# Kernel tuning notes

Hardware: AMD Instinct MI355X
Metric: run time of the kernel (lower is better)

Reference implementation:

```python
import jax, jax.numpy as jnp
import numpy as np

N_HEADS = 16

def setup_inputs() -> dict:
    key = jax.random.key(0)
    k1, k2, k3, k4, k5 = jax.random.split(key, 5)
    B, S, D = 2, 2048, 1024
    x = jax.random.normal(k1, (B, S, D), dtype=jnp.float32)
    # parameters scaled ~ fan-in to keep softmax logits sane
    w_in = jax.random.normal(k2, (D, 3 * D), dtype=jnp.float32) * (1.0 / np.sqrt(D))
    b_in = jax.random.normal(k3, (3 * D,), dtype=jnp.float32) * 0.02
    w_out = jax.random.normal(k4, (D, D), dtype=jnp.float32) * (1.0 / np.sqrt(D))
    b_out = jax.random.normal(k5, (D,), dtype=jnp.float32) * 0.02
    return {"x": x, "w_in": w_in, "b_in": b_in, "w_out": w_out, "b_out": b_out,
            "causal_mask": 1}


def reference(x, w_in, b_in, w_out, b_out, causal_mask):
    B, S, D = x.shape
    H = N_HEADS
    dh = D // H
    qkv = x @ w_in + b_in                        # [B, S, 3D]
    q, k, v = jnp.split(qkv, 3, axis=-1)          # each [B, S, D]
    q = q.reshape(B, S, H, dh)
    k = k.reshape(B, S, H, dh)
    v = v.reshape(B, S, H, dh)
    # scores: [B, H, Sq, Sk]
    scores = jnp.einsum("bqhd,bkhd->bhqk", q, k)
    if causal_mask:
        mask = jnp.triu(jnp.ones((S, S), dtype=bool), k=1)
        scores = jnp.where(mask, -jnp.inf, scores)
    scores = scores / jnp.sqrt(jnp.asarray(dh, dtype=scores.dtype))
    weight = jax.nn.softmax(scores, axis=-1)
    out = jnp.einsum("bhqk,bkhd->bqhd", weight, v).reshape(B, S, D)
    return out @ w_out + b_out
```

## Files before the change

### kernel.cpp

```cpp
#include <hip/hip_runtime.h>
#include <hip/hip_bf16.h>

typedef __attribute__((ext_vector_type(8))) short short8;
typedef __attribute__((ext_vector_type(4))) short s16x4;
typedef __attribute__((ext_vector_type(4))) float f32x4;
typedef unsigned short u16;

__device__ inline u16 f2bf(float f) {
    union { float f; unsigned u; } x{f};
    unsigned r = (x.u + 0x7fff + ((x.u >> 16) & 1)) >> 16;
    return (u16)r;
}

__device__ inline unsigned pkbf(float hi, float lo) {
    unsigned a = __builtin_bit_cast(unsigned, hi) + 0x8000u;
    unsigned b = __builtin_bit_cast(unsigned, lo) + 0x8000u;
    return __builtin_amdgcn_perm(a, b, 0x07060302u);
}

__device__ inline void glds16(const u16* g, u16* l) {
    __builtin_amdgcn_global_load_lds(
        (const __attribute__((address_space(1))) void*)g,
        (__attribute__((address_space(3))) void*)l, 16, 0, 0);
}

__global__ __launch_bounds__(256) void prep(const float* __restrict__ x,
                                            const float* __restrict__ w_in,
                                            const float* __restrict__ w_out,
                                            u16* __restrict__ Xb,
                                            u16* __restrict__ WtIn,
                                            u16* __restrict__ WtOut) {
    __shared__ float tile[32][33];
    int bx = blockIdx.x, tid = threadIdx.x;
    if (bx < 4096) {
        int i = (bx * 256 + tid) * 4;
        float4 v = *(const float4*)&x[i];
        uint2 o;
        o.x = (unsigned)f2bf(v.x) | ((unsigned)f2bf(v.y) << 16);
        o.y = (unsigned)f2bf(v.z) | ((unsigned)f2bf(v.w) << 16);
        *(uint2*)&Xb[i] = o;
        return;
    }
    const float* W; u16* Wt; int K, N, n0, k0;
    if (bx < 7168) {
        int b2 = bx - 4096;
        W = w_in; Wt = WtIn; K = 1024; N = 3072;
        n0 = (b2 % 96) * 32; k0 = (b2 / 96) * 32;
    } else {
        int b3 = bx - 7168;
        W = w_out; Wt = WtOut; K = 1024; N = 1024;
        n0 = (b3 & 31) * 32; k0 = (b3 >> 5) * 32;
    }
    int tx = tid & 31, ty = tid >> 5;
    for (int i = 0; i < 32; i += 8)
        tile[ty + i][tx] = W[(size_t)(k0 + ty + i) * N + n0 + tx];
    __syncthreads();
    for (int i = 0; i < 32; i += 8)
        Wt[(size_t)(n0 + ty + i) * K + k0 + tx] = f2bf(tile[tx][ty + i]);
}

__global__ __launch_bounds__(256) void transpose_v(const u16* __restrict__ qkv,
                                                   u16* __restrict__ VT) {
    __shared__ u16 t[32][33];
    int s0 = blockIdx.x * 32, d0 = blockIdx.y * 32, bh = blockIdx.z;
    int b = bh >> 4, h = bh & 15;
    int tx = threadIdx.x, ty = threadIdx.y;
    const u16* Vp = qkv + (size_t)(b * 2048) * 3072 + 2048 + h * 64;
    for (int i = 0; i < 32; i += 8)
        t[ty + i][tx] = Vp[(size_t)(s0 + ty + i) * 3072 + d0 + tx];
    __syncthreads();
    u16* Vr = VT + (size_t)bh * 64 * 2048;
    for (int i = 0; i < 32; i += 8)
        Vr[(size_t)(d0 + ty + i) * 2048 + s0 + tx] = t[tx][ty + i];
}

#define BM 128
#define BN 128
#define BK 64
__global__ __launch_bounds__(256) void gemm_bt(const u16* __restrict__ A,
                                               const u16* __restrict__ Bt,
                                               const float* __restrict__ bias,
                                               void* __restrict__ C,
                                               int M, int N, int K, int c_is_f32,
                                               int qcols, float qscale) {
    __shared__ u16 smem[2 * BM * BK + 2048];
    u16* As = smem;
    u16* Bs = smem + BM * BK;

    int tid = threadIdx.x;
    int wave = tid >> 6, lane = tid & 63;
    int quad = lane >> 4, l16 = lane & 15;
    int wm = (wave >> 1) * 64, wn = (wave & 1) * 64;

    int nm = M / BM, nn = N / BN;
    const int GM = 8;
    int per_group = GM * nn;
    int group = blockIdx.x / per_group;
    int rem = blockIdx.x % per_group;
    int first_m = group * GM;
    int gsz = (nm - first_m < GM) ? (nm - first_m) : GM;
    int m0 = (first_m + rem % gsz) * BM;
    int n0 = (rem / gsz) * BN;

    f32x4 acc[4][4] = {};

    for (int k0 = 0; k0 < K; k0 += BK) {
        __syncthreads();
        for (int i = 0; i < 4; i++) {
            int c = tid + i * 256;
            int r = c >> 3, cc = c & 7;
            int gsrc = (cc ^ (r & 7)) * 8;
            glds16(&A[(size_t)(m0 + r) * K + k0 + gsrc], As + c * 8);
            glds16(&Bt[(size_t)(n0 + r) * K + k0 + gsrc], Bs + c * 8);
        }
        __syncthreads();
        for (int ks = 0; ks < 2; ks++) {
            short8 af[4], bf[4];
            for (int i = 0; i < 4; i++) {
                int row = wm + i * 16 + l16;
                int slot = (ks * 4 + quad) ^ (row & 7);
                af[i] = *(short8*)&As[row * BK + slot * 8];
            }
            for (int j = 0; j < 4; j++) {
                int row = wn + j * 16 + l16;
                int slot = (ks * 4 + quad) ^ (row & 7);
                bf[j] = *(short8*)&Bs[row * BK + slot * 8];
            }
            for (int i = 0; i < 4; i++)
                for (int j = 0; j < 4; j++)
                    acc[i][j] = __builtin_amdgcn_mfma_f32_16x16x32_bf16(
                        af[i], bf[j], acc[i][j], 0, 0, 0);
        }
    }

    if (c_is_f32) {
        for (int i = 0; i < 4; i++)
            for (int j = 0; j < 4; j++) {
                int col = n0 + wn + j * 16 + l16;
                float bv = bias ? bias[col] : 0.f;
                for (int r = 0; r < 4; r++) {
                    int row = m0 + wm + i * 16 + quad * 4 + r;
                    ((float*)C)[(size_t)row * N + col] = acc[i][j][r] + bv;
                }
            }
    } else {
        __syncthreads();
        u16 (*buf)[136] = (u16(*)[136])smem;
        for (int i = 0; i < 4; i++)
            for (int j = 0; j < 4; j++) {
                int col = wn + j * 16 + l16;
                float bv = bias ? bias[n0 + col] : 0.f;
                float scl = (n0 + col < qcols) ? qscale : 1.f;
                for (int r = 0; r < 4; r++)
                    buf[wm + i * 16 + quad * 4 + r][col] =
                        f2bf((acc[i][j][r] + bv) * scl);
            }
        __syncthreads();
        u16* Cb = (u16*)C;
        for (int it = 0; it < 8; it++) {
            int c = tid + it * 256;
            int row = c >> 4, k8 = c & 15;
            uint4 v = *(uint4*)&buf[row][k8 * 8];
            *(uint4*)&Cb[(size_t)(m0 + row) * N + n0 + k8 * 8] = v;
        }
    }
}

__global__ __launch_bounds__(512) void attn_kernel(const u16* __restrict__ qkv,
                                                   const u16* __restrict__ VT,
                                                   u16* __restrict__ out) {
    const int S = 2048, D = 1024, stride = 3072;
    int idx = blockIdx.x;
    int p = idx >> 5, bh = idx & 31;
    int qtb[2] = {15 - p, p};
    int b = bh >> 4, h = bh & 15;
    int tid = threadIdx.x;
    int wave = tid >> 6, lane = tid & 63;
    int quad = lane >> 4, l16 = lane & 15;

    __shared__ u16 Klds[2][64 * 64];
    __shared__ u16 Vlds[2][64 * 64];
    __shared__ u16 Obuf[8][16][72];

    const u16* Qp = qkv + (size_t)(b * S) * stride + h * 64;
    const u16* Kp = Qp + D;
    const u16* Vtp = VT + (size_t)bh * 64 * S;

    short8 qf[2][2];
    for (int ph = 0; ph < 2; ph++) {
        int qrow = qtb[ph] * 128 + wave * 16 + l16;
        qf[ph][0] = *(const short8*)&Qp[(size_t)qrow * stride + quad * 8];
        qf[ph][1] = *(const short8*)&Qp[(size_t)qrow * stride + 32 + quad * 8];
    }

    int nt0 = 2 * qtb[0] + 2;
    int total = nt0 + 2 * qtb[1] + 2;

    auto stage = [&](int kt, int bsel) {
        int c = tid;
        int r = c >> 3, cc = c & 7;
        int gsrc = (cc ^ (r & 7)) * 8;
        glds16(&Kp[(size_t)(kt * 64 + r) * stride + gsrc], &Klds[bsel][c * 8]);
        glds16(&Vtp[(size_t)r * S + kt * 64 + gsrc], &Vlds[bsel][c * 8]);
    };

    stage(0, 0);

    f32x4 O[4] = {};
    float lsum = 0.f;

    for (int it = 0; it < total; it++) {
        int ph = (it >= nt0) ? 1 : 0;
        int kt = ph ? it - nt0 : it;
        int qt = qtb[ph];
        int cur = it & 1;
        __syncthreads();
        if (it + 1 < total) {
            int it2 = it + 1;
            int k2 = (it2 >= nt0) ? it2 - nt0 : it2;
            stage(k2, cur ^ 1);
        }

        short8 kf[4][2];
        for (int nb = 0; nb < 4; nb++) {
            int r = nb * 16 + l16;
            kf[nb][0] = *(short8*)&Klds[cur][r * 64 + ((0 + quad) ^ (r & 7)) * 8];
            kf[nb][1] = *(short8*)&Klds[cur][r * 64 + ((4 + quad) ^ (r & 7)) * 8];
        }
        f32x4 st[4];
        for (int nb = 0; nb < 4; nb++) {
            f32x4 t = {};
            t = __builtin_amdgcn_mfma_f32_16x16x32_bf16(kf[nb][0], qf[ph][0], t, 0, 0, 0);
            t = __builtin_amdgcn_mfma_f32_16x16x32_bf16(kf[nb][1], qf[ph][1], t, 0, 0, 0);
            st[nb] = t;
        }

        if (kt >= 2 * qt) {
            int qabs = qt * 128 + wave * 16 + l16;
            for (int nb = 0; nb < 4; nb++) {
                int kb = kt * 64 + nb * 16 + quad * 4;
                for (int r = 0; r < 4; r++) {
                    float e = __builtin_amdgcn_exp2f(st[nb][r]);
                    st[nb][r] = (kb + r <= qabs) ? e : 0.f;
                }
            }
        } else {
            for (int nb = 0; nb < 4; nb++)
                for (int r = 0; r < 4; r++)
                    st[nb][r] = __builtin_amdgcn_exp2f(st[nb][r]);
        }

        s16x4 pf[4];
        for (int nb = 0; nb < 4; nb++) {
            lsum += (st[nb][0] + st[nb][1]) + (st[nb][2] + st[nb][3]);
            uint2 pk;
            pk.x = pkbf(st[nb][1], st[nb][0]);
            pk.y = pkbf(st[nb][3], st[nb][2]);
            pf[nb] = __builtin_bit_cast(s16x4, pk);
        }

        for (int db = 0; db < 4; db++) {
            int rr = db * 16 + l16;
            for (int kc = 0; kc < 4; kc++) {
                int g = kc * 2 + (quad >> 1);
                int slot = g ^ (rr & 7);
                s16x4 vf = *(s16x4*)&Vlds[cur][rr * 64 + slot * 8 + (quad & 1) * 4];
                O[db] = __builtin_amdgcn_mfma_f32_16x16x16bf16_1k(
                    pf[kc], vf, O[db], 0, 0, 0);
            }
        }

        if (it == nt0 - 1 || it == total - 1) {
            float v = lsum;
            v += __shfl_xor(v, 16);
            v += __shfl_xor(v, 32);
            float rinv[4];
            for (int r = 0; r < 4; r++)
                rinv[r] = 1.f / __shfl(v, (lane & 48) | (quad * 4 + r));
            for (int db = 0; db < 4; db++)
                for (int r = 0; r < 4; r++)
                    Obuf[wave][quad * 4 + r][db * 16 + l16] =
                        f2bf(O[db][r] * rinv[r]);
            __asm__ volatile("s_waitcnt lgkmcnt(0)" ::: "memory");
            for (int i = 0; i < 2; i++) {
                int c = i * 64 + lane;
                int row = c >> 3, cc = c & 7;
                uint4 vv = *(uint4*)&Obuf[wave][row][cc * 8];
                int grow = qt * 128 + wave * 16 + row;
                *(uint4*)&out[(size_t)(b * S + grow) * D + h * 64 + cc * 8] = vv;
            }
            for (int db = 0; db < 4; db++) O[db] = (f32x4){0.f, 0.f, 0.f, 0.f};
            lsum = 0.f;
        }
    }
}

extern "C" void kernel_launch(void* const* d_in, const int* in_sizes, int n_in,
                              void* d_out, int out_size, void* d_ws, size_t ws_size,
                              hipStream_t stream) {
    const float* x     = (const float*)d_in[0];
    const float* w_in  = (const float*)d_in[1];
    const float* b_in  = (const float*)d_in[2];
    const float* w_out = (const float*)d_in[3];
    const float* b_out = (const float*)d_in[4];

    const int Bsz = 2, S = 2048, D = 1024, H = 16;
    const int M = Bsz * S;
    const int N1 = 3 * D;
    const float sc = 0.125f * 1.44269504f;

    u16* ws    = (u16*)d_ws;
    u16* Xb    = ws;
    u16* WtIn  = Xb + (size_t)M * D;
    u16* WtOut = WtIn + (size_t)N1 * D;
    u16* qkvb  = WtOut + (size_t)D * D;
    u16* attnb = qkvb + (size_t)M * N1;
    u16* Vt    = Xb;

    prep<<<8192, 256, 0, stream>>>(x, w_in, w_out, Xb, WtIn, WtOut);
    gemm_bt<<<(M / BM) * (N1 / BN), 256, 0, stream>>>(Xb, WtIn, b_in, qkvb,
                                                      M, N1, D, 0, D, sc);
    transpose_v<<<dim3(S / 32, 2, Bsz * H), dim3(32, 8), 0, stream>>>(qkvb, Vt);
    attn_kernel<<<256, 512, 0, stream>>>(qkvb, Vt, attnb);
    gemm_bt<<<(M / BM) * (D / BN), 256, 0, stream>>>(attnb, WtOut, b_out, d_out,
                                                     M, D, D, 1, 0, 1.f);
}
```

Before: 192.1 us.

## Process two K/V tiles per iteration in attention with dual accumulators

The attention loop now stages and consumes two 64-key tiles per iteration, using separate score, probability and output accumulators for each tile, and sums them at the end. This halves the number of barriers and gives the scheduler two independent MFMA chains to interleave, which should hide latency. It also adds a minimum-occupancy hint to launch bounds. The cost is doubled LDS (64KB+ for K/V) and more registers, which could lower occupancy or cause spills.

```diff
diff --git a/kernel.cpp b/kernel.cpp
--- a/kernel.cpp
+++ b/kernel.cpp
@@ -166,9 +166,9 @@
     }
 }
 
-__global__ __launch_bounds__(512) void attn_kernel(const u16* __restrict__ qkv,
-                                                   const u16* __restrict__ VT,
-                                                   u16* __restrict__ out) {
+__global__ __launch_bounds__(512, 2) void attn_kernel(const u16* __restrict__ qkv,
+                                                      const u16* __restrict__ VT,
+                                                      u16* __restrict__ out) {
     const int S = 2048, D = 1024, stride = 3072;
     int idx = blockIdx.x;
     int p = idx >> 5, bh = idx & 31;
@@ -178,8 +178,8 @@
     int wave = tid >> 6, lane = tid & 63;
     int quad = lane >> 4, l16 = lane & 15;
 
-    __shared__ u16 Klds[2][64 * 64];
-    __shared__ u16 Vlds[2][64 * 64];
+    __shared__ u16 Klds[2][2][64 * 64];
+    __shared__ u16 Vlds[2][2][64 * 64];
     __shared__ u16 Obuf[8][16][72];
 
     const u16* Qp = qkv + (size_t)(b * S) * stride + h * 64;
@@ -193,70 +193,90 @@
         qf[ph][1] = *(const short8*)&Qp[(size_t)qrow * stride + 32 + quad * 8];
     }
 
-    int nt0 = 2 * qtb[0] + 2;
-    int total = nt0 + 2 * qtb[1] + 2;
-
-    auto stage = [&](int kt, int bsel) {
+    int np0 = qtb[0] + 1;
+    int ntp = np0 + qtb[1] + 1;
+
+    auto stage = [&](int kt, int bsel, int ch) {
         int c = tid;
         int r = c >> 3, cc = c & 7;
         int gsrc = (cc ^ (r & 7)) * 8;
-        glds16(&Kp[(size_t)(kt * 64 + r) * stride + gsrc], &Klds[bsel][c * 8]);
-        glds16(&Vtp[(size_t)r * S + kt * 64 + gsrc], &Vlds[bsel][c * 8]);
+        glds16(&Kp[(size_t)(kt * 64 + r) * stride + gsrc], &Klds[bsel][ch][c * 8]);
+        glds16(&Vtp[(size_t)r * S + kt * 64 + gsrc], &Vlds[bsel][ch][c * 8]);
     };
 
-    stage(0, 0);
-
-    f32x4 O[4] = {};
-    float lsum = 0.f;
-
-    for (int it = 0; it < total; it++) {
-        int ph = (it >= nt0) ? 1 : 0;
-        int kt = ph ? it - nt0 : it;
+    stage(0, 0, 0);
+    stage(1, 0, 1);
+
+    f32x4 Oa[4] = {}, Ob[4] = {};
+    float lsa = 0.f, lsb = 0.f;
+
+    for (int jp = 0; jp < ntp; jp++) {
+        int ph = (jp >= np0) ? 1 : 0;
+        int j = ph ? jp - np0 : jp;
         int qt = qtb[ph];
-        int cur = it & 1;
-        __syncthreads();
-        if (it + 1 < total) {
-            int it2 = it + 1;
-            int k2 = (it2 >= nt0) ? it2 - nt0 : it2;
-            stage(k2, cur ^ 1);
-        }
-
-        short8 kf[4][2];
+        int ka = 2 * j, kb = 2 * j + 1;
+        int cur = jp & 1;
+        __syncthreads();
+        if (jp + 1 < ntp) {
+            int jp2 = jp + 1;
+            int j2 = (jp2 >= np0) ? jp2 - np0 : jp2;
+            stage(2 * j2, cur ^ 1, 0);
+            stage(2 * j2 + 1, cur ^ 1, 1);
+        }
+
+        short8 kfa[4][2], kfb[4][2];
         for (int nb = 0; nb < 4; nb++) {
             int r = nb * 16 + l16;
-            kf[nb][0] = *(short8*)&Klds[cur][r * 64 + ((0 + quad) ^ (r & 7)) * 8];
-            kf[nb][1] = *(short8*)&Klds[cur][r * 64 + ((4 + quad) ^ (r & 7)) * 8];
-        }
-        f32x4 st[4];
+            int s0 = ((0 + quad) ^ (r & 7)) * 8;
+            int s1 = ((4 + quad) ^ (r & 7)) * 8;
+            kfa[nb][0] = *(short8*)&Klds[cur][0][r * 64 + s0];
+            kfa[nb][1] = *(short8*)&Klds[cur][0][r * 64 + s1];
+            kfb[nb][0] = *(short8*)&Klds[cur][1][r * 64 + s0];
+            kfb[nb][1] = *(short8*)&Klds[cur][1][r * 64 + s1];
+        }
+        f32x4 sta[4], stb[4];
         for (int nb = 0; nb < 4; nb++) {
             f32x4 t = {};
-            t = __builtin_amdgcn_mfma_f32_16x16x32_bf16(kf[nb][0], qf[ph][0], t, 0, 0, 0);
-            t = __builtin_amdgcn_mfma_f32_16x16x32_bf16(kf[nb][1], qf[ph][1], t, 0, 0, 0);
-            st[nb] = t;
-        }
-
-        if (kt >= 2 * qt) {
+            t = __builtin_amdgcn_mfma_f32_16x16x32_bf16(kfa[nb][0], qf[ph][0], t, 0, 0, 0);
+            t = __builtin_amdgcn_mfma_f32_16x16x32_bf16(kfa[nb][1], qf[ph][1], t, 0, 0, 0);
+            sta[nb] = t;
+            f32x4 u = {};
+            u = __builtin_amdgcn_mfma_f32_16x16x32_bf16(kfb[nb][0], qf[ph][0], u, 0, 0, 0);
+            u = __builtin_amdgcn_mfma_f32_16x16x32_bf16(kfb[nb][1], qf[ph][1], u, 0, 0, 0);
+            stb[nb] = u;
+        }
+
+        if (j == qt) {
             int qabs = qt * 128 + wave * 16 + l16;
             for (int nb = 0; nb < 4; nb++) {
-                int kb = kt * 64 + nb * 16 + quad * 4;
+                int kba = ka * 64 + nb * 16 + quad * 4;
+                int kbb = kb * 64 + nb * 16 + quad * 4;
                 for (int r = 0; r < 4; r++) {
-                    float e = __builtin_amdgcn_exp2f(st[nb][r]);
-                    st[nb][r] = (kb + r <= qabs) ? e : 0.f;
+                    float ea = __builtin_amdgcn_exp2f(sta[nb][r]);
+                    sta[nb][r] = (kba + r <= qabs) ? ea : 0.f;
+                    float eb = __builtin_amdgcn_exp2f(stb[nb][r]);
+                    stb[nb][r] = (kbb + r <= qabs) ? eb : 0.f;
                 }
             }
         } else {
             for (int nb = 0; nb < 4; nb++)
-                for (int r = 0; r < 4; r++)
-                    st[nb][r] = __builtin_amdgcn_exp2f(st[nb][r]);
-        }
-
-        s16x4 pf[4];
+                for (int r = 0; r < 4; r++) {
+                    sta[nb][r] = __builtin_amdgcn_exp2f(sta[nb][r]);
+                    stb[nb][r] = __builtin_amdgcn_exp2f(stb[nb][r]);
+                }
+        }
+
+        s16x4 pfa[4], pfb[4];
         for (int nb = 0; nb < 4; nb++) {
-            lsum += (st[nb][0] + st[nb][1]) + (st[nb][2] + st[nb][3]);
+            lsa += (sta[nb][0] + sta[nb][1]) + (sta[nb][2] + sta[nb][3]);
+            lsb += (stb[nb][0] + stb[nb][1]) + (stb[nb][2] + stb[nb][3]);
             uint2 pk;
-            pk.x = pkbf(st[nb][1], st[nb][0]);
-            pk.y = pkbf(st[nb][3], st[nb][2]);
-            pf[nb] = __builtin_bit_cast(s16x4, pk);
+            pk.x = pkbf(sta[nb][1], sta[nb][0]);
+            pk.y = pkbf(sta[nb][3], sta[nb][2]);
+            pfa[nb] = __builtin_bit_cast(s16x4, pk);
+            pk.x = pkbf(stb[nb][1], stb[nb][0]);
+            pk.y = pkbf(stb[nb][3], stb[nb][2]);
+            pfb[nb] = __builtin_bit_cast(s16x4, pk);
         }
 
         for (int db = 0; db < 4; db++) {
@@ -264,14 +284,18 @@
             for (int kc = 0; kc < 4; kc++) {
                 int g = kc * 2 + (quad >> 1);
                 int slot = g ^ (rr & 7);
-                s16x4 vf = *(s16x4*)&Vlds[cur][rr * 64 + slot * 8 + (quad & 1) * 4];
-                O[db] = __builtin_amdgcn_mfma_f32_16x16x16bf16_1k(
-                    pf[kc], vf, O[db], 0, 0, 0);
-            }
-        }
-
-        if (it == nt0 - 1 || it == total - 1) {
-            float v = lsum;
+                int off = rr * 64 + slot * 8 + (quad & 1) * 4;
+                s16x4 vfa = *(s16x4*)&Vlds[cur][0][off];
+                Oa[db] = __builtin_amdgcn_mfma_f32_16x16x16bf16_1k(
+                    pfa[kc], vfa, Oa[db], 0, 0, 0);
+                s16x4 vfb = *(s16x4*)&Vlds[cur][1][off];
+                Ob[db] = __builtin_amdgcn_mfma_f32_16x16x16bf16_1k(
+                    pfb[kc], vfb, Ob[db], 0, 0, 0);
+            }
+        }
+
+        if (jp == np0 - 1 || jp == ntp - 1) {
+            float v = lsa + lsb;
             v += __shfl_xor(v, 16);
             v += __shfl_xor(v, 32);
             float rinv[4];
@@ -280,7 +304,7 @@
             for (int db = 0; db < 4; db++)
                 for (int r = 0; r < 4; r++)
                     Obuf[wave][quad * 4 + r][db * 16 + l16] =
-                        f2bf(O[db][r] * rinv[r]);
+                        f2bf((Oa[db][r] + Ob[db][r]) * rinv[r]);
             __asm__ volatile("s_waitcnt lgkmcnt(0)" ::: "memory");
             for (int i = 0; i < 2; i++) {
                 int c = i * 64 + lane;
@@ -289,8 +313,12 @@
                 int grow = qt * 128 + wave * 16 + row;
                 *(uint4*)&out[(size_t)(b * S + grow) * D + h * 64 + cc * 8] = vv;
             }
-            for (int db = 0; db < 4; db++) O[db] = (f32x4){0.f, 0.f, 0.f, 0.f};
-            lsum = 0.f;
+            for (int db = 0; db < 4; db++) {
+                Oa[db] = (f32x4){0.f, 0.f, 0.f, 0.f};
+                Ob[db] = (f32x4){0.f, 0.f, 0.f, 0.f};
+            }
+            lsa = 0.f;
+            lsb = 0.f;
         }
     }
 }
```

Measured after the change: 185.3 us. -3.5%, faster.
